# Kernel tuning notes

Measured on AMD Instinct MI355X. Metric: run time of the kernel, lower is better.

The kernel has to match this reference:

```python
import jax, jax.numpy as jnp
from jax import lax
import numpy as np

KERNEL = 3  # box filter size
D = 3       # displacement candidates per axis
SF = 2      # displacement stride


def _box_filter(x, pad):
    # grouped (depthwise) 3D conv with an all-ones k^3 kernel, stride 1
    C = x.shape[1]
    w = jnp.ones((C, 1, KERNEL, KERNEL, KERNEL), dtype=x.dtype)
    return lax.conv_general_dilated(
        x, w,
        window_strides=(1, 1, 1),
        padding=[(pad, pad)] * 3,
        dimension_numbers=("NCDHW", "OIDHW", "NCDHW"),
        feature_group_count=C,
    )


def setup_inputs() -> dict:
    key = jax.random.key(0)
    k1, k2 = jax.random.split(key)
    mov = jax.random.normal(k1, (1, 32, 96, 96, 96), dtype=jnp.float32)
    fix = jax.random.normal(k2, (1, 32, 96, 96, 96), dtype=jnp.float32)
    return {"mov": mov, "fix": fix}


def reference(mov, fix):
    B, C, H, W, T = mov.shape
    pm = _box_filter(mov, 1)        # [B,C,H,W,T]
    pf = _box_filter(fix, SF + 1)   # [B,C,H+4,W+4,T+4]
    outs = []
    for i in range(D):
        for j in range(D):
            for k in range(D):
                crop = lax.slice(
                    pf,
                    (0, 0, i * SF, j * SF, k * SF),
                    (B, C, i * SF + H, j * SF + W, k * SF + T),
                )
                outs.append(jnp.sum(pm * crop, axis=1))  # [B,H,W,T]
    corr = jnp.stack(outs, axis=1) / (KERNEL ** 3)  # [B,27,H,W,T]
    return corr
```

## Files before the change

kernel.cpp:

```cpp
#include <hip/hip_runtime.h>


#define CCH 32
#define HH  96
#define PP  100
#define TY  8
#define NZP 48
#define TPB (NZP * TY)
#define MST 104

__global__ __launch_bounds__(256) void pf1(const float* __restrict__ fix,
                                           float* __restrict__ pf) {
    int t = blockIdx.x * 256 + threadIdx.x;
    int oz = t % PP;
    int r  = t / PP;
    int oy = r % PP;
    r /= PP;
    int ox = r % PP;
    int c  = r / PP;

    int   szc[3];
    float zm[3];
#pragma unroll
    for (int m = 0; m < 3; ++m) {
        int s = oz - 3 + m;
        zm[m]  = ((unsigned)s < (unsigned)HH) ? 1.0f : 0.0f;
        szc[m] = min(max(s, 0), HH - 1);
    }

    float acc = 0.f;
#pragma unroll
    for (int a = 0; a < 3; ++a) {
        int sx = ox - 3 + a;
        if ((unsigned)sx >= (unsigned)HH) continue;
#pragma unroll
        for (int b = 0; b < 3; ++b) {
            int sy = oy - 3 + b;
            if ((unsigned)sy >= (unsigned)HH) continue;
            const float* row = fix + ((size_t)((c * HH + sx) * HH + sy)) * HH;
#pragma unroll
            for (int m = 0; m < 3; ++m)
                acc = fmaf(row[szc[m]], zm[m], acc);
        }
    }
    pf[((size_t)((c * PP + ox) * PP + oy)) * PP + oz] = acc;
}

__global__ __launch_bounds__(TPB) void corr2(const float* __restrict__ mov,
                                             const float* __restrict__ pf,
                                             float* __restrict__ out) {
    __shared__ float ms[3 * (TY + 2) * MST];
    __shared__ float ps[3 * (TY + 4) * MST];

    const int tid = threadIdx.x;
    const int zp  = tid % NZP;
    const int yy  = tid / NZP;
    const int bx  = blockIdx.x;
    const int y0  = blockIdx.y * TY;
    const int z0  = zp * 2;

    for (int s = tid; s < 3 * (TY + 2) * MST; s += TPB) ms[s] = 0.f;

    float acc[27][2];
#pragma unroll
    for (int d = 0; d < 27; ++d) { acc[d][0] = 0.f; acc[d][1] = 0.f; }

    const int NMS = 3 * (TY + 2) * (HH / 4);
    const int NPS = 3 * (TY + 4) * (PP / 4);

    for (int c = 0; c < CCH; ++c) {
        __syncthreads();
        for (int s = tid; s < NMS + NPS; s += TPB) {
            if (s < NMS) {
                int q = s % (HH / 4);
                int r = (s / (HH / 4)) % (TY + 2);
                int a = s / ((HH / 4) * (TY + 2));
                int sx = bx - 1 + a, sy = y0 - 1 + r;
                if ((unsigned)sx < (unsigned)HH && (unsigned)sy < (unsigned)HH) {
                    float4 v = *(const float4*)(
                        mov + ((size_t)((c * HH + sx) * HH + sy)) * HH + 4 * q);
                    *(float4*)(ms + (a * (TY + 2) + r) * MST + 4 + 4 * q) = v;
                }
            } else {
                int s2 = s - NMS;
                int q = s2 % (PP / 4);
                int r = (s2 / (PP / 4)) % (TY + 4);
                int i = s2 / ((PP / 4) * (TY + 4));
                int px = bx + 2 * i, py = y0 + r;
                float4 v = *(const float4*)(
                    pf + ((size_t)((c * PP + px) * PP + py)) * PP + 4 * q);
                *(float4*)(ps + (i * (TY + 4) + r) * MST + 4 * q) = v;
            }
        }
        __syncthreads();

        float b0 = 0.f, b1 = 0.f;
#pragma unroll
        for (int a = 0; a < 3; ++a)
#pragma unroll
            for (int b = 0; b < 3; ++b) {
                const float* col = ms + (a * (TY + 2) + (yy + b)) * MST + (z0 + 2);
                float2 u0 = *(const float2*)(col);
                float2 u1 = *(const float2*)(col + 2);
                float2 u2 = *(const float2*)(col + 4);
                b0 += u0.y + u1.x + u1.y;
                b1 += u1.x + u1.y + u2.x;
            }

#pragma unroll
        for (int i = 0; i < 3; ++i)
#pragma unroll
            for (int j = 0; j < 3; ++j) {
                const float* col = ps + (i * (TY + 4) + (yy + 2 * j)) * MST + z0;
                float2 w0 = *(const float2*)(col);
                float2 w1 = *(const float2*)(col + 2);
                float2 w2 = *(const float2*)(col + 4);
                int d = i * 9 + j * 3;
                acc[d][0]     = fmaf(b0, w0.x, acc[d][0]);
                acc[d][1]     = fmaf(b1, w0.y, acc[d][1]);
                acc[d + 1][0] = fmaf(b0, w1.x, acc[d + 1][0]);
                acc[d + 1][1] = fmaf(b1, w1.y, acc[d + 1][1]);
                acc[d + 2][0] = fmaf(b0, w2.x, acc[d + 2][0]);
                acc[d + 2][1] = fmaf(b1, w2.y, acc[d + 2][1]);
            }
    }

    const float sc = 1.0f / 27.0f;
    const int yo = y0 + yy;
#pragma unroll
    for (int d = 0; d < 27; ++d) {
        float2 o;
        o.x = acc[d][0] * sc;
        o.y = acc[d][1] * sc;
        *(float2*)(out + ((size_t)((d * HH + bx) * HH + yo)) * HH + z0) = o;
    }
}

extern "C" void kernel_launch(void* const* d_in, const int* in_sizes, int n_in,
                              void* d_out, int out_size, void* d_ws, size_t ws_size,
                              hipStream_t stream) {
    const float* mov = (const float*)d_in[0];
    const float* fix = (const float*)d_in[1];
    float* out = (float*)d_out;
    float* pf  = (float*)d_ws;

    if (ws_size < (size_t)CCH * PP * PP * PP * sizeof(float)) return;

    pf1<<<125000, 256, 0, stream>>>(fix, pf);

    corr2<<<dim3(96, 12), TPB, 0, stream>>>(mov, pf, out);
}
```

Baseline: 771.2 us.

## Vectorize box filter, pre-sum mov x-neighbors, four z outputs per thread

The fix box-filter kernel now computes four z outputs per thread from two float4 row loads and a sliding sum, with one float4 store. The correlation kernel sums the three x-neighbor planes of mov while loading to shared memory, so only one plane is staged. Each thread now computes four z outputs with float4 shared reads, and block indices are remapped in an interleaved order across tiles. This cuts redundant global and shared-memory traffic and per-output overhead, but doubles accumulator registers per thread (108) and halves the block size, which can lower occupancy.

Result: faster. 618.2 us (-19.8%).

```diff
diff --git a/kernel.cpp b/kernel.cpp
--- a/kernel.cpp
+++ b/kernel.cpp
@@ -5,30 +5,29 @@
 #define HH  96
 #define PP  100
 #define TY  8
-#define NZP 48
-#define TPB (NZP * TY)
+#define NZQ 24
+#define TPB (NZQ * TY)
 #define MST 104
 
-__global__ __launch_bounds__(256) void pf1(const float* __restrict__ fix,
+__global__ __launch_bounds__(256) void pf2(const float* __restrict__ fix,
                                            float* __restrict__ pf) {
     int t = blockIdx.x * 256 + threadIdx.x;
-    int oz = t % PP;
-    int r  = t / PP;
+    int q  = t % 25;
+    int r  = t / 25;
     int oy = r % PP;
     r /= PP;
     int ox = r % PP;
     int c  = r / PP;
+    int oz0 = q * 4;
 
-    int   szc[3];
-    float zm[3];
+    int baseA = max(oz0 - 4, 0);
+    int baseB = min(oz0, HH - 4);
+    float zm[6];
 #pragma unroll
-    for (int m = 0; m < 3; ++m) {
-        int s = oz - 3 + m;
-        zm[m]  = ((unsigned)s < (unsigned)HH) ? 1.0f : 0.0f;
-        szc[m] = min(max(s, 0), HH - 1);
-    }
+    for (int m = 0; m < 6; ++m)
+        zm[m] = ((unsigned)(oz0 - 3 + m) < (unsigned)HH) ? 1.0f : 0.0f;
 
-    float acc = 0.f;
+    float u0 = 0.f, u1 = 0.f, u2 = 0.f, u3 = 0.f, u4 = 0.f, u5 = 0.f;
 #pragma unroll
     for (int a = 0; a < 3; ++a) {
         int sx = ox - 3 + a;
@@ -38,54 +37,85 @@
             int sy = oy - 3 + b;
             if ((unsigned)sy >= (unsigned)HH) continue;
             const float* row = fix + ((size_t)((c * HH + sx) * HH + sy)) * HH;
-#pragma unroll
-            for (int m = 0; m < 3; ++m)
-                acc = fmaf(row[szc[m]], zm[m], acc);
+            float4 LA = *(const float4*)(row + baseA);
+            float4 LB = *(const float4*)(row + baseB);
+            u0 += LA.y; u1 += LA.z; u2 += LA.w;
+            u3 += LB.x; u4 += LB.y; u5 += LB.z;
         }
     }
-    pf[((size_t)((c * PP + ox) * PP + oy)) * PP + oz] = acc;
+    u0 *= zm[0]; u1 *= zm[1]; u2 *= zm[2];
+    u3 *= zm[3]; u4 *= zm[4]; u5 *= zm[5];
+
+    float4 o;
+    o.x = u0 + u1 + u2;
+    o.y = u1 + u2 + u3;
+    o.z = u2 + u3 + u4;
+    o.w = u3 + u4 + u5;
+    *(float4*)(pf + ((size_t)((c * PP + ox) * PP + oy)) * PP + oz0) = o;
 }
 
-__global__ __launch_bounds__(TPB) void corr2(const float* __restrict__ mov,
+__global__ __launch_bounds__(TPB) void corr3(const float* __restrict__ mov,
                                              const float* __restrict__ pf,
                                              float* __restrict__ out) {
-    __shared__ float ms[3 * (TY + 2) * MST];
+    __shared__ float xs[(TY + 2) * MST];
     __shared__ float ps[3 * (TY + 4) * MST];
 
     const int tid = threadIdx.x;
-    const int zp  = tid % NZP;
-    const int yy  = tid / NZP;
-    const int bx  = blockIdx.x;
-    const int y0  = blockIdx.y * TY;
-    const int z0  = zp * 2;
+    const int zq  = tid % NZQ;
+    const int yy  = tid / NZQ;
+    const int z0  = zq * 4;
 
-    for (int s = tid; s < 3 * (TY + 2) * MST; s += TPB) ms[s] = 0.f;
+    const int bid = blockIdx.x;
+    const int tile = (bid & 7) * 144 + (bid >> 3);
+    const int bx = tile % 96;
+    const int by = tile / 96;
+    const int y0 = by * TY;
 
-    float acc[27][2];
+    for (int s = tid; s < (TY + 2) * MST; s += TPB) xs[s] = 0.f;
+
+    float acc[27][4];
 #pragma unroll
-    for (int d = 0; d < 27; ++d) { acc[d][0] = 0.f; acc[d][1] = 0.f; }
+    for (int d = 0; d < 27; ++d)
+#pragma unroll
+        for (int qq = 0; qq < 4; ++qq) acc[d][qq] = 0.f;
 
-    const int NMS = 3 * (TY + 2) * (HH / 4);
+    const int NXS = (TY + 2) * (HH / 4);
     const int NPS = 3 * (TY + 4) * (PP / 4);
+
+    const bool xlo = (bx >= 1), xhi = (bx <= HH - 2);
 
     for (int c = 0; c < CCH; ++c) {
         __syncthreads();
-        for (int s = tid; s < NMS + NPS; s += TPB) {
-            if (s < NMS) {
+        for (int s = tid; s < NXS + NPS; s += TPB) {
+            if (s < NXS) {
                 int q = s % (HH / 4);
-                int r = (s / (HH / 4)) % (TY + 2);
-                int a = s / ((HH / 4) * (TY + 2));
-                int sx = bx - 1 + a, sy = y0 - 1 + r;
-                if ((unsigned)sx < (unsigned)HH && (unsigned)sy < (unsigned)HH) {
-                    float4 v = *(const float4*)(
-                        mov + ((size_t)((c * HH + sx) * HH + sy)) * HH + 4 * q);
-                    *(float4*)(ms + (a * (TY + 2) + r) * MST + 4 + 4 * q) = v;
+                int r = s / (HH / 4);
+                int sy = y0 - 1 + r;
+                float4 v = {0.f, 0.f, 0.f, 0.f};
+                if ((unsigned)sy < (unsigned)HH) {
+                    const float* base =
+                        mov + ((size_t)(c * HH + bx) * HH + sy) * HH + 4 * q;
+                    const size_t pstr = (size_t)HH * HH;
+                    if (xlo) {
+                        float4 a = *(const float4*)(base - pstr);
+                        v.x += a.x; v.y += a.y; v.z += a.z; v.w += a.w;
+                    }
+                    {
+                        float4 a = *(const float4*)(base);
+                        v.x += a.x; v.y += a.y; v.z += a.z; v.w += a.w;
+                    }
+                    if (xhi) {
+                        float4 a = *(const float4*)(base + pstr);
+                        v.x += a.x; v.y += a.y; v.z += a.z; v.w += a.w;
+                    }
                 }
+                *(float4*)(xs + r * MST + 4 + 4 * q) = v;
             } else {
-                int s2 = s - NMS;
-                int q = s2 % (PP / 4);
-                int r = (s2 / (PP / 4)) % (TY + 4);
-                int i = s2 / ((PP / 4) * (TY + 4));
+                int s2 = s - NXS;
+                int q  = s2 % (PP / 4);
+                int rr = s2 / (PP / 4);
+                int r  = rr % (TY + 4);
+                int i  = rr / (TY + 4);
                 int px = bx + 2 * i, py = y0 + r;
                 float4 v = *(const float4*)(
                     pf + ((size_t)((c * PP + px) * PP + py)) * PP + 4 * q);
@@ -94,34 +124,36 @@
         }
         __syncthreads();
 
-        float b0 = 0.f, b1 = 0.f;
+        float bmv[4] = {0.f, 0.f, 0.f, 0.f};
 #pragma unroll
-        for (int a = 0; a < 3; ++a)
-#pragma unroll
-            for (int b = 0; b < 3; ++b) {
-                const float* col = ms + (a * (TY + 2) + (yy + b)) * MST + (z0 + 2);
-                float2 u0 = *(const float2*)(col);
-                float2 u1 = *(const float2*)(col + 2);
-                float2 u2 = *(const float2*)(col + 4);
-                b0 += u0.y + u1.x + u1.y;
-                b1 += u1.x + u1.y + u2.x;
-            }
+        for (int b = 0; b < 3; ++b) {
+            const float* col = xs + (yy + b) * MST + z0 + 2;
+            float2 e0 = *(const float2*)(col);
+            float2 e1 = *(const float2*)(col + 2);
+            float2 e2 = *(const float2*)(col + 4);
+            float2 e3 = *(const float2*)(col + 6);
+            bmv[0] += e0.y + e1.x + e1.y;
+            bmv[1] += e1.x + e1.y + e2.x;
+            bmv[2] += e1.y + e2.x + e2.y;
+            bmv[3] += e2.x + e2.y + e3.x;
+        }
 
 #pragma unroll
         for (int i = 0; i < 3; ++i)
 #pragma unroll
             for (int j = 0; j < 3; ++j) {
-                const float* col = ps + (i * (TY + 4) + (yy + 2 * j)) * MST + z0;
-                float2 w0 = *(const float2*)(col);
-                float2 w1 = *(const float2*)(col + 2);
-                float2 w2 = *(const float2*)(col + 4);
-                int d = i * 9 + j * 3;
-                acc[d][0]     = fmaf(b0, w0.x, acc[d][0]);
-                acc[d][1]     = fmaf(b1, w0.y, acc[d][1]);
-                acc[d + 1][0] = fmaf(b0, w1.x, acc[d + 1][0]);
-                acc[d + 1][1] = fmaf(b1, w1.y, acc[d + 1][1]);
-                acc[d + 2][0] = fmaf(b0, w2.x, acc[d + 2][0]);
-                acc[d + 2][1] = fmaf(b1, w2.y, acc[d + 2][1]);
+                const float* col =
+                    ps + (i * (TY + 4) + (yy + 2 * j)) * MST + z0;
+                float4 w0 = *(const float4*)(col);
+                float4 w1 = *(const float4*)(col + 4);
+                float w[8] = {w0.x, w0.y, w0.z, w0.w, w1.x, w1.y, w1.z, w1.w};
+#pragma unroll
+                for (int k = 0; k < 3; ++k) {
+                    int d = i * 9 + j * 3 + k;
+#pragma unroll
+                    for (int qq = 0; qq < 4; ++qq)
+                        acc[d][qq] = fmaf(bmv[qq], w[qq + 2 * k], acc[d][qq]);
+                }
             }
     }
 
@@ -129,10 +161,12 @@
     const int yo = y0 + yy;
 #pragma unroll
     for (int d = 0; d < 27; ++d) {
-        float2 o;
+        float4 o;
         o.x = acc[d][0] * sc;
         o.y = acc[d][1] * sc;
-        *(float2*)(out + ((size_t)((d * HH + bx) * HH + yo)) * HH + z0) = o;
+        o.z = acc[d][2] * sc;
+        o.w = acc[d][3] * sc;
+        *(float4*)(out + ((size_t)((d * HH + bx) * HH + yo)) * HH + z0) = o;
     }
 }
 
@@ -146,7 +180,7 @@
 
     if (ws_size < (size_t)CCH * PP * PP * PP * sizeof(float)) return;
 
-    pf1<<<125000, 256, 0, stream>>>(fix, pf);
+    pf2<<<31250, 256, 0, stream>>>(fix, pf);
 
-    corr2<<<dim3(96, 12), TPB, 0, stream>>>(mov, pf, out);
+    corr3<<<1152, TPB, 0, stream>>>(mov, pf, out);
 }
```
